# Performance work log

Hardware: AMD Instinct MI355X
Metric: run time of the kernel (lower is better)

## Reference

```python
import jax, jax.numpy as jnp
import numpy as np

B, N, H = 2, 1024, 768
MAX_W = 30
WIDTH_D = 20
SPAN_DIM = 3 * H + WIDTH_D  # 2324
K = int(N * 0.4)  # 409 (eval mode: // (1+0) )


def _enumerate_spans(n, max_w):
    # Replicates: enumerate_spans then sorted(spans[::-1], key=start)
    # -> start ascending, end DESCENDING within each start.
    spans = []
    for s in range(n):
        for e in range(min(s + max_w - 1, n - 1), s - 1, -1):
            spans.append((s, e))
    return np.asarray(spans, dtype=np.int32)  # [num_spans, 2]


def setup_inputs() -> dict:
    key = jax.random.key(0)
    ks = jax.random.split(key, 8)
    spans = jnp.asarray(_enumerate_spans(N, MAX_W))  # [30285, 2]
    return {
        "segment_embeddings": jax.random.normal(ks[0], (B, N, H), jnp.float32),
        "segment_mask": jnp.ones((B, N), jnp.int32),
        "candidate_spans": spans,
        "width_emb": jax.random.normal(ks[1], (MAX_W, WIDTH_D), jnp.float32) * 0.02,
        "W1": jax.random.normal(ks[2], (SPAN_DIM, H), jnp.float32) * 0.02,
        "b1": jax.random.normal(ks[3], (H,), jnp.float32) * 0.02,
        "w_s": jax.random.normal(ks[4], (H,), jnp.float32) * 0.02,
        "b_s": jax.random.normal(ks[5], (1,), jnp.float32) * 0.02,
        "k": K,
    }


def reference(segment_embeddings, segment_mask, candidate_spans, width_emb, W1, b1, w_s, b_s, k):
    starts = candidate_spans[:, 0]  # [S]
    ends = candidate_spans[:, 1]    # [S]
    # Endpoint span extractor: x, y, x*y + width embedding (width = end-start)
    x = segment_embeddings[:, starts, :]          # [B,S,H]
    y = segment_embeddings[:, ends, :]            # [B,S,H]
    wemb = width_emb[ends - starts]               # [S,WIDTH_D]
    bsz = segment_embeddings.shape[0]
    span_feat = jnp.concatenate(
        [x, y, x * y, jnp.broadcast_to(wemb[None], (bsz,) + wemb.shape)], axis=-1
    )  # [B,S,3H+WD]
    # MLP (dropout is identity in eval) + GELU (torch default: exact erf)
    h = jax.nn.gelu(jnp.einsum("bsd,dh->bsh", span_feat, W1) + b1, approximate=False)
    scores = jnp.einsum("bsh,h->bs", h, w_s) + b_s[0]  # [B,S]
    # Mask spans whose end index exceeds valid length
    lengths = segment_mask.sum(-1)  # [B]
    scores = scores + jnp.where(ends[None, :] >= lengths[:, None], -1e6, 0.0)
    # Top-k prune, then sort indices and gather
    _, idx = jax.lax.top_k(scores, k)          # [B,k]
    idx = jnp.sort(idx, axis=1)
    top_scores = jnp.take_along_axis(scores, idx, axis=1)            # [B,k]
    top_span_embs = jnp.take_along_axis(h, idx[:, :, None], axis=1)  # [B,k,H]
    top_spans = candidate_spans[idx]                                 # [B,k,2]
    return top_span_embs, top_scores, top_spans
```

## Files before the change

### kernel.cpp

```cpp
#include <hip/hip_runtime.h>
#include <math.h>

#define NB 2
#define NN 1024
#define HH 768
#define MAXW 30
#define KTOP 409
#define BANDCAP 4096
#define BAND_TAU 2e-2f
#define FILTCAP 6144
#define GROWS 512

typedef __attribute__((ext_vector_type(4))) float f32x4;
typedef __attribute__((ext_vector_type(8))) __bf16 bf16x8;
typedef __attribute__((ext_vector_type(8))) unsigned short us8;

__device__ __forceinline__ float gelu_f(float z) {
  return 0.5f * z * (1.0f + erff(z * 0.70710678118654752440f));
}
__device__ __forceinline__ unsigned f2key(float f) {
  unsigned u = __float_as_uint(f);
  return (u & 0x80000000u) ? ~u : (u | 0x80000000u);
}
__device__ __forceinline__ float key2f(unsigned k) {
  unsigned u = (k & 0x80000000u) ? (k & 0x7fffffffu) : ~k;
  return __uint_as_float(u);
}
__device__ __forceinline__ unsigned short f2bf_rn(float f) {
  unsigned u = __float_as_uint(f);
  unsigned r = u + 0x7fffu + ((u >> 16) & 1u);
  return (unsigned short)(r >> 16);
}
__device__ __forceinline__ float bf2f(unsigned short h) {
  return __uint_as_float(((unsigned)h) << 16);
}
__device__ __forceinline__ void async_copy16(const void* g, void* l) {
  __builtin_amdgcn_global_load_lds(
      (const __attribute__((address_space(1))) unsigned int*)g,
      (__attribute__((address_space(3))) unsigned int*)l, 16, 0, 0);
}

__global__ void len_kernel(const int* __restrict__ mask, int* __restrict__ lengths) {
  __shared__ int red[256];
  for (int b = 0; b < NB; ++b) {
    int s = 0;
    for (int i = threadIdx.x; i < NN; i += 256) s += mask[b * NN + i];
    red[threadIdx.x] = s;
    __syncthreads();
    for (int off = 128; off > 0; off >>= 1) {
      if (threadIdx.x < off) red[threadIdx.x] += red[threadIdx.x + off];
      __syncthreads();
    }
    if (threadIdx.x == 0) lengths[b] = red[0];
    __syncthreads();
  }
}

__global__ void r_kernel(const float* __restrict__ wemb, const float* __restrict__ W1,
                         const float* __restrict__ b1, float* __restrict__ R) {
  int w = blockIdx.x;
  for (int h = threadIdx.x; h < HH; h += 256) {
    float acc = b1[h];
    for (int j = 0; j < 20; ++j)
      acc = fmaf(wemb[w * 20 + j], W1[(size_t)(3 * HH + j) * HH + h], acc);
    R[w * HH + h] = acc;
  }
}

__global__ __launch_bounds__(256) void prep_bt_kernel(const float* __restrict__ W1,
                                                      unsigned short* __restrict__ Bt,
                                                      unsigned short* __restrict__ Btlo) {
  const int ki = blockIdx.x;
  const int hby = blockIdx.y;
  const float* W1c = W1 + (size_t)(2 * HH) * HH;
  const int t = threadIdx.x;
#pragma unroll
  for (int half = 0; half < 2; ++half) {
    const int c = t + half * 256;
    const int col = c >> 2, kg = c & 3;
    us8 hv, lv;
#pragma unroll
    for (int j = 0; j < 8; ++j) {
      const int k = ki * 32 + kg * 8 + j;
      float v = W1c[(size_t)k * HH + hby * 128 + col];
      unsigned short h = f2bf_rn(v);
      hv[j] = h;
      lv[j] = f2bf_rn(v - bf2f(h));
    }
    const size_t bo = ((size_t)(hby * 24 + ki) * 512 + c) * 8;
    *(us8*)(Bt + bo) = hv;
    *(us8*)(Btlo + bo) = lv;
  }
}

__global__ __launch_bounds__(256) void prep_emb_hl_kernel(
    const float* __restrict__ emb, unsigned short* __restrict__ Ahi,
    unsigned short* __restrict__ Alo) {
  const int tile = blockIdx.x;
  const int ki = blockIdx.y;
  const int t = threadIdx.x;
#pragma unroll
  for (int half = 0; half < 2; ++half) {
    const int c = t + half * 256;
    const int row = c >> 2, kgs = c & 3;
    const int kg = kgs ^ ((row >> 1) & 3);
    const float* xr = emb + (size_t)(tile * 128 + row) * HH;
    const int k0 = ki * 32 + kg * 8;
    float4 x0 = *(const float4*)(xr + k0);
    float4 x1 = *(const float4*)(xr + k0 + 4);
    const float xv[8] = {x0.x, x0.y, x0.z, x0.w, x1.x, x1.y, x1.z, x1.w};
    us8 hv, lv;
#pragma unroll
    for (int j = 0; j < 8; ++j) {
      unsigned short h = f2bf_rn(xv[j]);
      hv[j] = h;
      lv[j] = f2bf_rn(xv[j] - bf2f(h));
    }
    const size_t base = (((size_t)tile * 24 + ki) * 512 + c) * 8;
    *(us8*)(Ahi + base) = hv;
    *(us8*)(Alo + base) = lv;
  }
}

__global__ __launch_bounds__(256) void prep_w1ab_kernel(
    const float* __restrict__ W1, unsigned short* __restrict__ Bhi,
    unsigned short* __restrict__ Blo) {
  const int ki = blockIdx.x;
  const int hby = blockIdx.y;
  const int t = threadIdx.x;
#pragma unroll
  for (int half = 0; half < 2; ++half) {
    const int c = t + half * 256;
    const int col = c >> 2, kg = c & 3;
    const int gc = hby * 128 + col;
    const float* base = W1 + (gc < 768 ? (size_t)0 : (size_t)HH * HH);
    const int n = (gc < 768) ? gc : gc - 768;
    us8 hv, lv;
#pragma unroll
    for (int j = 0; j < 8; ++j) {
      const int k = ki * 32 + kg * 8 + j;
      float v = base[(size_t)k * HH + n];
      unsigned short h = f2bf_rn(v);
      hv[j] = h;
      lv[j] = f2bf_rn(v - bf2f(h));
    }
    const size_t bo = (((size_t)hby * 24 + ki) * 512 + c) * 8;
    *(us8*)(Bhi + bo) = hv;
    *(us8*)(Blo + bo) = lv;
  }
}

__global__ __launch_bounds__(256) void pq_mfma_kernel(
    const unsigned short* __restrict__ Ahi, const unsigned short* __restrict__ Alo,
    const unsigned short* __restrict__ Bhi, const unsigned short* __restrict__ Blo,
    float* __restrict__ P, float* __restrict__ Q) {
  __shared__ unsigned short AsmH[128 * 32], AsmL[128 * 32];
  const int tile = blockIdx.x;
  const int hby = blockIdx.y;
  const int tid = threadIdx.x;
  const int lane = tid & 63, w = tid >> 6;
  const int wm = w & 1, wn = w >> 1;
  const int lm = lane & 15, lq = lane >> 4;

  f32x4 acc[4][4];
#pragma unroll
  for (int i = 0; i < 4; ++i)
#pragma unroll
    for (int j = 0; j < 4; ++j) acc[i][j] = (f32x4){0.f, 0.f, 0.f, 0.f};

  const unsigned short* AbH = Ahi + (size_t)tile * 24 * 4096;
  const unsigned short* AbL = Alo + (size_t)tile * 24 * 4096;
  const unsigned short* BbH = Bhi + (size_t)hby * 24 * 4096;
  const unsigned short* BbL = Blo + (size_t)hby * 24 * 4096;
  const int a_off = (wm * 64 + lm) * 32 + (lq ^ ((lm >> 1) & 3)) * 8;
  const int b_off = (wn * 64 + lm) * 32 + lq * 8;

  for (int ki = 0; ki < 24; ++ki) {
    async_copy16(AbH + (size_t)ki * 4096 + tid * 8, AsmH + tid * 8);
    async_copy16(AbH + (size_t)ki * 4096 + (tid + 256) * 8, AsmH + (tid + 256) * 8);
    async_copy16(AbL + (size_t)ki * 4096 + tid * 8, AsmL + tid * 8);
    async_copy16(AbL + (size_t)ki * 4096 + (tid + 256) * 8, AsmL + (tid + 256) * 8);
    bf16x8 bh[4], bl[4];
#pragma unroll
    for (int ni = 0; ni < 4; ++ni) {
      bh[ni] = *reinterpret_cast<const bf16x8*>(BbH + (size_t)ki * 4096 + b_off + ni * 512);
      bl[ni] = *reinterpret_cast<const bf16x8*>(BbL + (size_t)ki * 4096 + b_off + ni * 512);
    }
    __syncthreads();
    bf16x8 ah[4], al[4];
#pragma unroll
    for (int mi = 0; mi < 4; ++mi) {
      ah[mi] = *reinterpret_cast<const bf16x8*>(AsmH + a_off + mi * 512);
      al[mi] = *reinterpret_cast<const bf16x8*>(AsmL + a_off + mi * 512);
    }
#pragma unroll
    for (int ni = 0; ni < 4; ++ni)
#pragma unroll
      for (int mi = 0; mi < 4; ++mi) {
        acc[mi][ni] = __builtin_amdgcn_mfma_f32_16x16x32_bf16(ah[mi], bh[ni], acc[mi][ni], 0, 0, 0);
        acc[mi][ni] = __builtin_amdgcn_mfma_f32_16x16x32_bf16(ah[mi], bl[ni], acc[mi][ni], 0, 0, 0);
        acc[mi][ni] = __builtin_amdgcn_mfma_f32_16x16x32_bf16(al[mi], bh[ni], acc[mi][ni], 0, 0, 0);
      }
    __syncthreads();
  }

  float* Obase = (hby < 6) ? P : Q;
  const int cb = ((hby < 6) ? hby : hby - 6) * 128 + wn * 64 + lm;
  const int rowb = tile * 128 + wm * 64 + lq * 4;
#pragma unroll
  for (int mi = 0; mi < 4; ++mi)
#pragma unroll
    for (int ni = 0; ni < 4; ++ni)
#pragma unroll
      for (int r = 0; r < 4; ++r)
        Obase[(size_t)(rowb + mi * 16 + r) * HH + cb + ni * 16] = acc[mi][ni][r];
}

__global__ __launch_bounds__(512, 4) void score_mfma6_kernel(
    const float* __restrict__ emb, const int* __restrict__ spans,
    const unsigned short* __restrict__ Bt, const float* __restrict__ w_s,
    const float* __restrict__ P, const float* __restrict__ Q, const float* __restrict__ R,
    float* __restrict__ spart, int S) {
  __shared__ unsigned short Asm[128 * 32];
  __shared__ int ssm[128], eem[128], wwm[128];
  __shared__ float sred[128 * 4];

  const int colblk = blockIdx.x;
  const int tile = blockIdx.y;
  const int b = blockIdx.z;
  const int tid = threadIdx.x;
  const int lane = tid & 63, w = tid >> 6;
  const int wm = w & 1, wn = w >> 1;
  const int lm = lane & 15, lq = lane >> 4;

  if (tid < 128) {
    int g = tile * 128 + tid;
    int gg = g < S ? g : S - 1;
    int s = spans[2 * gg], e = spans[2 * gg + 1];
    ssm[tid] = s; eem[tid] = e; wwm[tid] = e - s;
  }
  __syncthreads();

  const int arow = tid >> 2;
  const int kgs = tid & 3;
  const int kg = kgs ^ ((arow >> 1) & 3);
  const float* xr = emb + ((size_t)b * NN + ssm[arow]) * HH;
  const float* yr = emb + ((size_t)b * NN + eem[arow]) * HH;
  const int aw_off = (arow * 4 + kgs) * 8;

  f32x4 acc[4][4];
#pragma unroll
  for (int i = 0; i < 4; ++i)
#pragma unroll
    for (int j = 0; j < 4; ++j) acc[i][j] = (f32x4){0.f, 0.f, 0.f, 0.f};

  const int hby = colblk * 2 + (wn >> 1);
  const unsigned short* Bb = Bt + (size_t)hby * 24 * 4096;
  const int b_off = ((wn & 1) * 64 + lm) * 32 + lq * 8;
  const int a_off = (wm * 64 + lm) * 32 + (lq ^ ((lm >> 1) & 3)) * 8;

  for (int ki = 0; ki < 24; ++ki) {
    const int k0 = ki * 32 + kg * 8;
    float4 x0 = *(const float4*)(xr + k0);
    float4 x1 = *(const float4*)(xr + k0 + 4);
    float4 y0 = *(const float4*)(yr + k0);
    float4 y1 = *(const float4*)(yr + k0 + 4);
    us8 v;
    v[0] = f2bf_rn(x0.x * y0.x); v[1] = f2bf_rn(x0.y * y0.y);
    v[2] = f2bf_rn(x0.z * y0.z); v[3] = f2bf_rn(x0.w * y0.w);
    v[4] = f2bf_rn(x1.x * y1.x); v[5] = f2bf_rn(x1.y * y1.y);
    v[6] = f2bf_rn(x1.z * y1.z); v[7] = f2bf_rn(x1.w * y1.w);
    __syncthreads();
    *(us8*)(Asm + aw_off) = v;
    __syncthreads();
    bf16x8 afr[4];
#pragma unroll
    for (int mi = 0; mi < 4; ++mi)
      afr[mi] = *reinterpret_cast<const bf16x8*>(Asm + a_off + mi * 512);
#pragma unroll
    for (int ni = 0; ni < 4; ++ni) {
      bf16x8 bfr = *reinterpret_cast<const bf16x8*>(Bb + (size_t)ki * 4096 + b_off + ni * 512);
#pragma unroll
      for (int mi = 0; mi < 4; ++mi)
        acc[mi][ni] = __builtin_amdgcn_mfma_f32_16x16x32_bf16(afr[mi], bfr, acc[mi][ni], 0, 0, 0);
    }
  }

  const int cbase = colblk * 256 + wn * 64 + lm;
  float wsv[4];
#pragma unroll
  for (int ni = 0; ni < 4; ++ni) wsv[ni] = w_s[cbase + ni * 16];

#pragma unroll
  for (int mi = 0; mi < 4; ++mi) {
#pragma unroll
    for (int r = 0; r < 4; ++r) {
      const int rowl = wm * 64 + mi * 16 + lq * 4 + r;
      const int s = ssm[rowl], e = eem[rowl], wd = wwm[rowl];
      const float* Pp = P + ((size_t)b * NN + s) * HH + cbase;
      const float* Qp = Q + ((size_t)b * NN + e) * HH + cbase;
      const float* Rp = R + (size_t)wd * HH + cbase;
      float psum = 0.f;
#pragma unroll
      for (int ni = 0; ni < 4; ++ni) {
        float z = acc[mi][ni][r] + Pp[ni * 16] + Qp[ni * 16] + Rp[ni * 16];
        psum = fmaf(gelu_f(z), wsv[ni], psum);
      }
      psum += __shfl_xor(psum, 1);
      psum += __shfl_xor(psum, 2);
      psum += __shfl_xor(psum, 4);
      psum += __shfl_xor(psum, 8);
      if (lm == 0) sred[rowl * 4 + wn] = psum;
    }
  }
  __syncthreads();
  if (tid < 128) {
    int g = tile * 128 + tid;
    if (g < S)
      spart[(size_t)colblk * ((size_t)NB * S) + (size_t)b * S + g] =
          sred[tid * 4] + sred[tid * 4 + 1] + sred[tid * 4 + 2] + sred[tid * 4 + 3];
  }
}

__global__ void combine_kernel(const float* __restrict__ sp, const int* __restrict__ spans,
                               const float* __restrict__ b_s, const int* __restrict__ lengths,
                               float* __restrict__ scores, int S) {
  int idx = blockIdx.x * 256 + threadIdx.x;
  if (idx >= NB * S) return;
  int b = idx / S, i = idx - b * S;
  size_t st = (size_t)NB * S;
  float v = b_s[0];
#pragma unroll
  for (int j = 0; j < 3; ++j) v += sp[j * st + idx];
  if (spans[2 * i + 1] >= lengths[b]) v += -1000000.0f;
  scores[idx] = v;
}

__global__ void zero_kernel(unsigned* __restrict__ hist, int* __restrict__ bandcount,
                            int* __restrict__ filtcount) {
  int i = blockIdx.x * 256 + threadIdx.x;
  hist[i] = 0;
  if (blockIdx.x == 0 && threadIdx.x < NB) {
    bandcount[threadIdx.x] = 0;
    filtcount[threadIdx.x] = 0;
  }
}

__global__ void hist16_kernel(const float* __restrict__ scores, unsigned* __restrict__ hist,
                              int S) {
  int idx = blockIdx.x * 256 + threadIdx.x;
  if (idx >= NB * S) return;
  int b = idx / S;
  unsigned key = f2key(scores[idx]) >> 16;
  atomicAdd(&hist[(size_t)b * 65536 + key], 1u);
}

__global__ __launch_bounds__(1024) void scan16_kernel(const unsigned* __restrict__ hist,
                                                      const int* __restrict__ kptr,
                                                      float* __restrict__ pivotf) {
  const int b = blockIdx.x;
  const unsigned* hb = hist + (size_t)b * 65536;
  const int tid = threadIdx.x;
  const unsigned k = (unsigned)kptr[0];
  __shared__ unsigned acc[1024];
  unsigned s = 0;
  for (int j = 0; j < 64; ++j) s += hb[tid * 64 + j];
  const unsigned mysum = s;
  acc[tid] = s;
  __syncthreads();
  for (int off = 1; off < 1024; off <<= 1) {
    unsigned v = (tid + off < 1024) ? acc[tid + off] : 0u;
    __syncthreads();
    acc[tid] += v;
    __syncthreads();
  }
  const unsigned above = acc[tid] - mysum;
  if (above < k && acc[tid] >= k) {
    unsigned cum = above;
    int binf = tid * 64;
    for (int j = 63; j >= 0; --j) {
      unsigned c = hb[tid * 64 + j];
      if (cum + c >= k) { binf = tid * 64 + j; break; }
      cum += c;
    }
    pivotf[b] = key2f(((unsigned)binf) << 16);
  }
}

__global__ void band_kernel(const float* __restrict__ scores, const float* __restrict__ pivotf,
                            int* __restrict__ bandcount, int* __restrict__ bandlist, int S) {
  int idx = blockIdx.x * 256 + threadIdx.x;
  if (idx >= NB * S) return;
  int b = idx / S, i = idx - b * S;
  if (fabsf(scores[idx] - pivotf[b]) <= BAND_TAU) {
    int slot = atomicAdd(&bandcount[b], 1);
    if (slot < BANDCAP) bandlist[b * BANDCAP + slot] = i;
  }
}

__global__ __launch_bounds__(256) void rescore_kernel(
    const float* __restrict__ emb, const int* __restrict__ spans,
    const float* __restrict__ W1, const float* __restrict__ w_s,
    const float* __restrict__ b_s, const int* __restrict__ lengths,
    const float* __restrict__ P, const float* __restrict__ Q, const float* __restrict__ R,
    const int* __restrict__ bandcount, const int* __restrict__ bandlist,
    float* __restrict__ scores, int S) {
  const int b = blockIdx.y;
  int cnt = bandcount[b];
  if (cnt > BANDCAP) cnt = BANDCAP;
  if ((int)blockIdx.x >= cnt) return;
  const int i = bandlist[b * BANDCAP + blockIdx.x];
  const int s = spans[2 * i], e = spans[2 * i + 1], wd = e - s;
  const int tid = threadIdx.x;
  __shared__ float prod[HH];
  __shared__ float red[256];
  for (int c = tid; c < HH; c += 256)
    prod[c] = emb[((size_t)b * NN + s) * HH + c] * emb[((size_t)b * NN + e) * HH + c];
  __syncthreads();
  const float* W1c = W1 + (size_t)(2 * HH) * HH;
  float psum = 0.f;
  for (int c0 = 0; c0 < HH; c0 += 256) {
    const int c = c0 + tid;
    float a = P[((size_t)b * NN + s) * HH + c] + Q[((size_t)b * NN + e) * HH + c] + R[(size_t)wd * HH + c];
    for (int k = 0; k < HH; ++k) a = fmaf(prod[k], W1c[(size_t)k * HH + c], a);
    psum = fmaf(gelu_f(a), w_s[c], psum);
  }
  red[tid] = psum;
  __syncthreads();
  for (int off = 128; off > 0; off >>= 1) {
    if (tid < off) red[tid] += red[tid + off];
    __syncthreads();
  }
  if (tid == 0) {
    float v = red[0] + b_s[0];
    if (e >= lengths[b]) v += -1000000.0f;
    scores[(size_t)b * S + i] = v;
  }
}

__global__ void filt_kernel(const float* __restrict__ scores, const float* __restrict__ pivotf,
                            int* __restrict__ filtcount, int* __restrict__ filtlist, int S) {
  int idx = blockIdx.x * 256 + threadIdx.x;
  if (idx >= NB * S) return;
  int b = idx / S, i = idx - b * S;
  if (scores[idx] > pivotf[b] - 0.01f) {
    int slot = atomicAdd(&filtcount[b], 1);
    if (slot < FILTCAP) filtlist[b * FILTCAP + slot] = i;
  }
}

__global__ __launch_bounds__(1024) void sel_kernel(
    const float* __restrict__ scores, const int* __restrict__ spans,
    const int* __restrict__ kptr, const int* __restrict__ filtcount,
    const int* __restrict__ filtlist,
    float* __restrict__ out_spans, int* __restrict__ sel, int S) {
  const int b = blockIdx.x;
  const int tid = threadIdx.x;
  const int k = kptr[0];
  __shared__ unsigned keys[FILTCAP];
  __shared__ int idxs[FILTCAP];
  __shared__ unsigned hist[256];
  __shared__ unsigned sh_prefix;
  __shared__ int sh_remaining;
  __shared__ int selcnt;
  __shared__ int slist[512];

  int M = filtcount[b];
  if (M > FILTCAP) M = FILTCAP;
  for (int i = tid; i < M; i += 1024) {
    int gi = filtlist[b * FILTCAP + i];
    idxs[i] = gi;
    keys[i] = f2key(scores[(size_t)b * S + gi]);
  }
  if (tid == 0) selcnt = 0;
  __syncthreads();

  unsigned prefix = 0;
  int remaining = k;
  for (int round = 0; round < 4; ++round) {
    const int shift = 24 - 8 * round;
    if (tid < 256) hist[tid] = 0;
    __syncthreads();
    for (int i = tid; i < M; i += 1024) {
      unsigned key = keys[i];
      if (round == 0 || (key >> (shift + 8)) == prefix)
        atomicAdd(&hist[(key >> shift) & 255u], 1u);
    }
    __syncthreads();
    if (tid == 0) {
      int cum = 0;
      for (int bin = 255; bin >= 0; --bin) {
        int c = (int)hist[bin];
        if (cum + c >= remaining) {
          sh_prefix = (prefix << 8) | (unsigned)bin;
          sh_remaining = remaining - cum;
          break;
        }
        cum += c;
      }
    }
    __syncthreads();
    prefix = sh_prefix;
    remaining = sh_remaining;
    __syncthreads();
  }
  const unsigned pk = prefix;
  const int m_eq = remaining;

  for (int i = tid; i < M; i += 1024) {
    unsigned key = keys[i];
    bool pick = false;
    if (key > pk) {
      pick = true;
    } else if (key == pk) {
      int r = 0;
      const int myidx = idxs[i];
      for (int j = 0; j < M; ++j)
        if (keys[j] == pk && idxs[j] < myidx) ++r;
      pick = (r < m_eq);
    }
    if (pick) {
      int p = atomicAdd(&selcnt, 1);
      if (p < 512) slist[p] = idxs[i];
    }
  }
  __syncthreads();

  for (int i = tid; i < k; i += 1024) {
    const int my = slist[i];
    int r = 0;
    for (int j = 0; j < k; ++j) r += (slist[j] < my);
    sel[b * KTOP + r] = my;
    out_spans[(b * KTOP + r) * 2 + 0] = (float)spans[2 * my];
    out_spans[(b * KTOP + r) * 2 + 1] = (float)spans[2 * my + 1];
  }
}

__global__ __launch_bounds__(256) void prep_ga_kernel(
    const float* __restrict__ emb, const int* __restrict__ spans,
    const int* __restrict__ sel, unsigned short* __restrict__ GAhi,
    unsigned short* __restrict__ GAlo) {
  const int bx = blockIdx.x;
  const int tile = bx / 24, ki = bx - tile * 24;
  const int b = blockIdx.y;
  const int t = threadIdx.x;
#pragma unroll
  for (int half = 0; half < 2; ++half) {
    const int c = t + half * 256;
    const int row = c >> 2, kgs = c & 3;
    const int kg = kgs ^ ((row >> 1) & 3);
    int j = tile * 128 + row;
    if (j >= KTOP) j = KTOP - 1;
    const int i = sel[b * KTOP + j];
    const int s = spans[2 * i], e = spans[2 * i + 1];
    const float* xr = emb + ((size_t)b * NN + s) * HH;
    const float* yr = emb + ((size_t)b * NN + e) * HH;
    const int k0 = ki * 32 + kg * 8;
    float4 x0 = *(const float4*)(xr + k0);
    float4 x1 = *(const float4*)(xr + k0 + 4);
    float4 y0 = *(const float4*)(yr + k0);
    float4 y1 = *(const float4*)(yr + k0 + 4);
    const float pv[8] = {x0.x * y0.x, x0.y * y0.y, x0.z * y0.z, x0.w * y0.w,
                         x1.x * y1.x, x1.y * y1.y, x1.z * y1.z, x1.w * y1.w};
    us8 hv, lv;
#pragma unroll
    for (int q = 0; q < 8; ++q) {
      unsigned short h = f2bf_rn(pv[q]);
      hv[q] = h;
      lv[q] = f2bf_rn(pv[q] - bf2f(h));
    }
    const size_t base = (((size_t)(b * 4 + tile) * 24 + ki) * 512 + c) * 8;
    *(us8*)(GAhi + base) = hv;
    *(us8*)(GAlo + base) = lv;
  }
}

__global__ __launch_bounds__(256) void gather_mfma_kernel(
    const int* __restrict__ spans, const int* __restrict__ sel,
    const unsigned short* __restrict__ GAhi, const unsigned short* __restrict__ GAlo,
    const unsigned short* __restrict__ Bt, const unsigned short* __restrict__ Btlo,
    const float* __restrict__ w_s,
    const float* __restrict__ P, const float* __restrict__ Q, const float* __restrict__ R,
    float* __restrict__ outh, float* __restrict__ spartg) {
  __shared__ unsigned short AsmH[128 * 32], AsmL[128 * 32];
  __shared__ int ssm[128], eem[128], wwm[128], vvm[128];
  __shared__ float sred[128 * 2];
  const int tile = blockIdx.x;
  const int hby = blockIdx.y;
  const int b = blockIdx.z;
  const int tid = threadIdx.x;
  const int lane = tid & 63, w = tid >> 6;
  const int wm = w & 1, wn = w >> 1;
  const int lm = lane & 15, lq = lane >> 4;

  if (tid < 128) {
    int j = tile * 128 + tid;
    int valid = (j < KTOP) ? 1 : 0;
    int jj = valid ? j : KTOP - 1;
    int i = sel[b * KTOP + jj];
    ssm[tid] = spans[2 * i];
    eem[tid] = spans[2 * i + 1];
    wwm[tid] = eem[tid] - ssm[tid];
    vvm[tid] = valid;
  }

  f32x4 acc[4][4];
#pragma unroll
  for (int i = 0; i < 4; ++i)
#pragma unroll
    for (int j = 0; j < 4; ++j) acc[i][j] = (f32x4){0.f, 0.f, 0.f, 0.f};

  const unsigned short* AbH = GAhi + (size_t)(b * 4 + tile) * 24 * 4096;
  const unsigned short* AbL = GAlo + (size_t)(b * 4 + tile) * 24 * 4096;
  const unsigned short* BbH = Bt + (size_t)hby * 24 * 4096;
  const unsigned short* BbL = Btlo + (size_t)hby * 24 * 4096;
  const int a_off = (wm * 64 + lm) * 32 + (lq ^ ((lm >> 1) & 3)) * 8;
  const int b_off = (wn * 64 + lm) * 32 + lq * 8;

  for (int ki = 0; ki < 24; ++ki) {
    async_copy16(AbH + (size_t)ki * 4096 + tid * 8, AsmH + tid * 8);
    async_copy16(AbH + (size_t)ki * 4096 + (tid + 256) * 8, AsmH + (tid + 256) * 8);
    async_copy16(AbL + (size_t)ki * 4096 + tid * 8, AsmL + tid * 8);
    async_copy16(AbL + (size_t)ki * 4096 + (tid + 256) * 8, AsmL + (tid + 256) * 8);
    bf16x8 bh[4], bl[4];
#pragma unroll
    for (int ni = 0; ni < 4; ++ni) {
      bh[ni] = *reinterpret_cast<const bf16x8*>(BbH + (size_t)ki * 4096 + b_off + ni * 512);
      bl[ni] = *reinterpret_cast<const bf16x8*>(BbL + (size_t)ki * 4096 + b_off + ni * 512);
    }
    __syncthreads();
    bf16x8 ah[4], al[4];
#pragma unroll
    for (int mi = 0; mi < 4; ++mi) {
      ah[mi] = *reinterpret_cast<const bf16x8*>(AsmH + a_off + mi * 512);
      al[mi] = *reinterpret_cast<const bf16x8*>(AsmL + a_off + mi * 512);
    }
#pragma unroll
    for (int ni = 0; ni < 4; ++ni)
#pragma unroll
      for (int mi = 0; mi < 4; ++mi) {
        acc[mi][ni] = __builtin_amdgcn_mfma_f32_16x16x32_bf16(ah[mi], bh[ni], acc[mi][ni], 0, 0, 0);
        acc[mi][ni] = __builtin_amdgcn_mfma_f32_16x16x32_bf16(ah[mi], bl[ni], acc[mi][ni], 0, 0, 0);
        acc[mi][ni] = __builtin_amdgcn_mfma_f32_16x16x32_bf16(al[mi], bh[ni], acc[mi][ni], 0, 0, 0);
      }
    __syncthreads();
  }

  const int hbg = hby * 128;
  float wsv[4];
#pragma unroll
  for (int ni = 0; ni < 4; ++ni) wsv[ni] = w_s[hbg + wn * 64 + ni * 16 + lm];

#pragma unroll
  for (int mi = 0; mi < 4; ++mi) {
#pragma unroll
    for (int r = 0; r < 4; ++r) {
      const int rowl = wm * 64 + mi * 16 + lq * 4 + r;
      const int s = ssm[rowl], e = eem[rowl], wd = wwm[rowl];
      const float* Pp = P + ((size_t)b * NN + s) * HH + hbg + wn * 64 + lm;
      const float* Qp = Q + ((size_t)b * NN + e) * HH + hbg + wn * 64 + lm;
      const float* Rp = R + (size_t)wd * HH + hbg + wn * 64 + lm;
      float psum = 0.f;
      const int j = tile * 128 + rowl;
      float* op = outh + (size_t)(b * KTOP + j) * HH + hbg + wn * 64 + lm;
#pragma unroll
      for (int ni = 0; ni < 4; ++ni) {
        float z = acc[mi][ni][r] + Pp[ni * 16] + Qp[ni * 16] + Rp[ni * 16];
        float gl = gelu_f(z);
        if (vvm[rowl]) op[ni * 16] = gl;
        psum = fmaf(gl, wsv[ni], psum);
      }
      psum += __shfl_xor(psum, 1);
      psum += __shfl_xor(psum, 2);
      psum += __shfl_xor(psum, 4);
      psum += __shfl_xor(psum, 8);
      if (lm == 0) sred[rowl * 2 + wn] = psum;
    }
  }
  __syncthreads();
  if (tid < 128)
    spartg[(size_t)hby * (NB * GROWS) + b * GROWS + tile * 128 + tid] =
        sred[tid * 2] + sred[tid * 2 + 1];
}

__global__ void score_fin_kernel(const float* __restrict__ spartg, const int* __restrict__ sel,
                                 const int* __restrict__ spans, const float* __restrict__ b_s,
                                 const int* __restrict__ lengths, float* __restrict__ out_scores) {
  int idx = blockIdx.x * 256 + threadIdx.x;
  if (idx >= NB * KTOP) return;
  int b = idx / KTOP, j = idx - b * KTOP;
  float v = b_s[0];
#pragma unroll
  for (int hby = 0; hby < 6; ++hby)
    v += spartg[(size_t)hby * (NB * GROWS) + b * GROWS + j];
  int i = sel[idx];
  if (spans[2 * i + 1] >= lengths[b]) v += -1000000.0f;
  out_scores[idx] = v;
}

extern "C" void kernel_launch(void* const* d_in, const int* in_sizes, int n_in,
                              void* d_out, int out_size, void* d_ws, size_t ws_size,
                              hipStream_t stream) {
  const float* emb = (const float*)d_in[0];
  const int* mask = (const int*)d_in[1];
  const int* spans = (const int*)d_in[2];
  const float* wemb = (const float*)d_in[3];
  const float* W1 = (const float*)d_in[4];
  const float* b1 = (const float*)d_in[5];
  const float* w_s = (const float*)d_in[6];
  const float* b_s = (const float*)d_in[7];
  const int* kptr = (const int*)d_in[8];
  const int S = in_sizes[2] / 2;
  float* out = (float*)d_out;

  char* wp = (char*)d_ws;
  auto take = [&](size_t bytes) {
    char* p = wp;
    wp += (bytes + 63) & ~(size_t)63;
    return p;
  };
  float* Pb = (float*)take((size_t)NB * NN * HH * 4);
  float* Qb = (float*)take((size_t)NB * NN * HH * 4);
  float* Rb = (float*)take((size_t)MAXW * HH * 4);
  float* spart = (float*)take(3 * (size_t)NB * S * 4);
  float* scoresb = (float*)take((size_t)NB * S * 4);
  float* spartg = (float*)take(6 * (size_t)NB * GROWS * 4);
  float* pivotf = (float*)take(NB * 4);
  unsigned short* AimgHi = (unsigned short*)take((size_t)16 * 24 * 4096 * 2);
  unsigned short* AimgLo = (unsigned short*)take((size_t)16 * 24 * 4096 * 2);
  unsigned short* BimgHi = (unsigned short*)take((size_t)12 * 24 * 4096 * 2);
  unsigned short* BimgLo = (unsigned short*)take((size_t)12 * 24 * 4096 * 2);
  unsigned short* Bt = (unsigned short*)take((size_t)6 * 24 * 4096 * 2);
  unsigned short* Btlo = (unsigned short*)take((size_t)6 * 24 * 4096 * 2);
  unsigned short* GAhi = (unsigned short*)take((size_t)NB * 4 * 24 * 4096 * 2);
  unsigned short* GAlo = (unsigned short*)take((size_t)NB * 4 * 24 * 4096 * 2);
  unsigned* hist16b = (unsigned*)take((size_t)NB * 65536 * 4);
  int* selb = (int*)take(NB * KTOP * 4);
  int* lengthsb = (int*)take(NB * 4);
  int* bandcount = (int*)take(NB * 4);
  int* bandlist = (int*)take((size_t)NB * BANDCAP * 4);
  int* filtcount = (int*)take(NB * 4);
  int* filtlist = (int*)take((size_t)NB * FILTCAP * 4);

  const size_t OFF1 = (size_t)NB * KTOP * HH;
  const size_t OFF2 = OFF1 + (size_t)NB * KTOP;

  const int tiles = (S + 127) / 128;

  len_kernel<<<dim3(1), dim3(256), 0, stream>>>(mask, lengthsb);
  r_kernel<<<dim3(MAXW), dim3(256), 0, stream>>>(wemb, W1, b1, Rb);
  prep_bt_kernel<<<dim3(24, 6), dim3(256), 0, stream>>>(W1, Bt, Btlo);
  prep_emb_hl_kernel<<<dim3(16, 24), dim3(256), 0, stream>>>(emb, AimgHi, AimgLo);
  prep_w1ab_kernel<<<dim3(24, 12), dim3(256), 0, stream>>>(W1, BimgHi, BimgLo);
  pq_mfma_kernel<<<dim3(16, 12), dim3(256), 0, stream>>>(AimgHi, AimgLo, BimgHi, BimgLo, Pb, Qb);
  zero_kernel<<<dim3(512), dim3(256), 0, stream>>>(hist16b, bandcount, filtcount);

  score_mfma6_kernel<<<dim3(3, tiles, NB), dim3(512), 0, stream>>>(
      emb, spans, Bt, w_s, Pb, Qb, Rb, spart, S);

  combine_kernel<<<dim3((NB * S + 255) / 256), dim3(256), 0, stream>>>(
      spart, spans, b_s, lengthsb, scoresb, S);
  hist16_kernel<<<dim3((NB * S + 255) / 256), dim3(256), 0, stream>>>(scoresb, hist16b, S);
  scan16_kernel<<<dim3(NB), dim3(1024), 0, stream>>>(hist16b, kptr, pivotf);
  band_kernel<<<dim3((NB * S + 255) / 256), dim3(256), 0, stream>>>(
      scoresb, pivotf, bandcount, bandlist, S);
  rescore_kernel<<<dim3(BANDCAP, NB), dim3(256), 0, stream>>>(
      emb, spans, W1, w_s, b_s, lengthsb, Pb, Qb, Rb, bandcount, bandlist, scoresb, S);
  filt_kernel<<<dim3((NB * S + 255) / 256), dim3(256), 0, stream>>>(
      scoresb, pivotf, filtcount, filtlist, S);
  sel_kernel<<<dim3(NB), dim3(1024), 0, stream>>>(
      scoresb, spans, kptr, filtcount, filtlist, out + OFF2, selb, S);
  prep_ga_kernel<<<dim3(96, NB), dim3(256), 0, stream>>>(emb, spans, selb, GAhi, GAlo);
  gather_mfma_kernel<<<dim3(4, 6, NB), dim3(256), 0, stream>>>(
      spans, selb, GAhi, GAlo, Bt, Btlo, w_s, Pb, Qb, Rb, out, spartg);
  score_fin_kernel<<<dim3((NB * KTOP + 255) / 256), dim3(256), 0, stream>>>(
      spartg, selb, spans, b_s, lengthsb, out + OFF1);
}
```

Measured before the change: 550.0 us.

## Stage the tile's embedding row window in double-buffered LDS for the x*y product

The score kernel now computes the min start and max end over the 128 spans in a tile and stages that contiguous window of embedding rows (capped at 40) into a double-buffered shared-memory slab, one 32-column chunk per k-step, with register prefetch two steps ahead. Each thread then reads its start and end rows from LDS instead of issuing scattered global loads per span, which removes redundant global traffic because many spans share rows. The cost is more shared memory and a serial 128-element reduction on one thread. The cap also silently clamps the window, so a tile spanning more than 40 rows would read wrong data; that cannot happen for the sorted span list with width 30.

```diff
diff --git a/kernel.cpp b/kernel.cpp
--- a/kernel.cpp
+++ b/kernel.cpp
@@ -10,6 +10,7 @@
 #define BAND_TAU 2e-2f
 #define FILTCAP 6144
 #define GROWS 512
+#define WCAP 40
 
 typedef __attribute__((ext_vector_type(4))) float f32x4;
 typedef __attribute__((ext_vector_type(8))) __bf16 bf16x8;
@@ -216,14 +217,16 @@
         Obase[(size_t)(rowb + mi * 16 + r) * HH + cb + ni * 16] = acc[mi][ni][r];
 }
 
-__global__ __launch_bounds__(512, 4) void score_mfma6_kernel(
+__global__ __launch_bounds__(512, 4) void score_mfma7_kernel(
     const float* __restrict__ emb, const int* __restrict__ spans,
     const unsigned short* __restrict__ Bt, const float* __restrict__ w_s,
     const float* __restrict__ P, const float* __restrict__ Q, const float* __restrict__ R,
     float* __restrict__ spart, int S) {
   __shared__ unsigned short Asm[128 * 32];
+  __shared__ float ew[2][WCAP * 32];
   __shared__ int ssm[128], eem[128], wwm[128];
   __shared__ float sred[128 * 4];
+  __shared__ int rminS, rmaxS;
 
   const int colblk = blockIdx.x;
   const int tile = blockIdx.y;
@@ -240,12 +243,29 @@
     ssm[tid] = s; eem[tid] = e; wwm[tid] = e - s;
   }
   __syncthreads();
+  if (tid == 0) {
+    int rmn = ssm[0], rmx = eem[0];
+    for (int i = 1; i < 128; ++i) {
+      rmn = min(rmn, ssm[i]);
+      rmx = max(rmx, eem[i]);
+    }
+    rminS = rmn; rmaxS = rmx;
+  }
+  __syncthreads();
+  const int rmin = rminS;
+  int W = rmaxS - rmin + 1;
+  if (W > WCAP) W = WCAP;
+
+  const int sr = tid >> 3, sc = (tid & 7) * 4;
+  const bool stager = (tid < W * 8);
+  const float* gsrc = emb + ((size_t)b * NN + rmin + sr) * HH + sc;
+  const int ewoff = sr * 32 + sc;
 
   const int arow = tid >> 2;
   const int kgs = tid & 3;
   const int kg = kgs ^ ((arow >> 1) & 3);
-  const float* xr = emb + ((size_t)b * NN + ssm[arow]) * HH;
-  const float* yr = emb + ((size_t)b * NN + eem[arow]) * HH;
+  const int xo = (ssm[arow] - rmin) * 32 + kg * 8;
+  const int yo = (eem[arow] - rmin) * 32 + kg * 8;
   const int aw_off = (arow * 4 + kgs) * 8;
 
   f32x4 acc[4][4];
@@ -259,20 +279,30 @@
   const int b_off = ((wn & 1) * 64 + lm) * 32 + lq * 8;
   const int a_off = (wm * 64 + lm) * 32 + (lq ^ ((lm >> 1) & 3)) * 8;
 
+  float4 reg = make_float4(0.f, 0.f, 0.f, 0.f);
+  if (stager) {
+    float4 r0 = *(const float4*)gsrc;
+    *(float4*)(&ew[0][ewoff]) = r0;
+    reg = *(const float4*)(gsrc + 32);
+  }
+  __syncthreads();
+
+  int cur = 0;
   for (int ki = 0; ki < 24; ++ki) {
-    const int k0 = ki * 32 + kg * 8;
-    float4 x0 = *(const float4*)(xr + k0);
-    float4 x1 = *(const float4*)(xr + k0 + 4);
-    float4 y0 = *(const float4*)(yr + k0);
-    float4 y1 = *(const float4*)(yr + k0 + 4);
+    float4 x0 = *(const float4*)(&ew[cur][xo]);
+    float4 x1 = *(const float4*)(&ew[cur][xo + 4]);
+    float4 y0 = *(const float4*)(&ew[cur][yo]);
+    float4 y1 = *(const float4*)(&ew[cur][yo + 4]);
     us8 v;
     v[0] = f2bf_rn(x0.x * y0.x); v[1] = f2bf_rn(x0.y * y0.y);
     v[2] = f2bf_rn(x0.z * y0.z); v[3] = f2bf_rn(x0.w * y0.w);
     v[4] = f2bf_rn(x1.x * y1.x); v[5] = f2bf_rn(x1.y * y1.y);
     v[6] = f2bf_rn(x1.z * y1.z); v[7] = f2bf_rn(x1.w * y1.w);
-    __syncthreads();
     *(us8*)(Asm + aw_off) = v;
-    __syncthreads();
+    if (stager && ki < 23) *(float4*)(&ew[1 - cur][ewoff]) = reg;
+    __syncthreads();
+    if (stager && ki + 2 < 24)
+      reg = *(const float4*)(gsrc + (size_t)(ki + 2) * 32);
     bf16x8 afr[4];
 #pragma unroll
     for (int mi = 0; mi < 4; ++mi)
@@ -284,6 +314,8 @@
       for (int mi = 0; mi < 4; ++mi)
         acc[mi][ni] = __builtin_amdgcn_mfma_f32_16x16x32_bf16(afr[mi], bfr, acc[mi][ni], 0, 0, 0);
     }
+    __syncthreads();
+    cur ^= 1;
   }
 
   const int cbase = colblk * 256 + wn * 64 + lm;
@@ -755,7 +787,7 @@
   pq_mfma_kernel<<<dim3(16, 12), dim3(256), 0, stream>>>(AimgHi, AimgLo, BimgHi, BimgLo, Pb, Qb);
   zero_kernel<<<dim3(512), dim3(256), 0, stream>>>(hist16b, bandcount, filtcount);
 
-  score_mfma6_kernel<<<dim3(3, tiles, NB), dim3(512), 0, stream>>>(
+  score_mfma7_kernel<<<dim3(3, tiles, NB), dim3(512), 0, stream>>>(
       emb, spans, Bt, w_s, Pb, Qb, Rb, spart, S);
 
   combine_kernel<<<dim3((NB * S + 255) / 256), dim3(256), 0, stream>>>(
```

Result: no change. 546.1 us (-0.7%).
